# Kernel tuning notes

Measured on AMD Instinct MI355X. Metric: run time of the kernel, lower is better.

Reference implementation:

```python
import jax, jax.numpy as jnp
import numpy as np

# ---- JPEG constants ----
_Y_TABLE = np.array([
    [16, 11, 10, 16, 24, 40, 51, 61],
    [12, 12, 14, 19, 26, 58, 60, 55],
    [14, 13, 16, 24, 40, 57, 69, 56],
    [14, 17, 22, 29, 51, 87, 80, 62],
    [18, 22, 37, 56, 68, 109, 103, 77],
    [24, 35, 55, 64, 81, 104, 113, 92],
    [49, 64, 78, 87, 103, 121, 120, 101],
    [72, 92, 95, 98, 112, 100, 103, 99]], dtype=np.float32)
_C_TABLE = np.full((8, 8), 99.0, dtype=np.float32)
_C_TABLE[:4, :4] = np.array([
    [17, 18, 24, 47],
    [18, 21, 26, 66],
    [24, 26, 56, 99],
    [47, 66, 99, 99]], dtype=np.float32)

_i = np.arange(8, dtype=np.float64)
_T = (np.cos((2 * _i[:, None, None, None] + 1) * _i[None, None, :, None] * np.pi / 16)
      * np.cos((2 * _i[None, :, None, None] + 1) * _i[None, None, None, :] * np.pi / 16))
_alpha = np.ones(8); _alpha[0] = 1.0 / np.sqrt(2.0)
DCT_T = jnp.asarray(_T, jnp.float32)
DCT_SCALE = jnp.asarray(np.outer(_alpha, _alpha) * 0.25, jnp.float32)
IDCT_ALPHA = jnp.asarray(np.outer(_alpha, _alpha), jnp.float32)
Y_T = jnp.asarray(_Y_TABLE)
C_T = jnp.asarray(_C_TABLE)


def _split_blocks(c):
    # [N,H,W] -> [N, (H//8)*(W//8), 8, 8]
    N, H, W = c.shape
    return c.reshape(N, H // 8, 8, W // 8, 8).transpose(0, 1, 3, 2, 4).reshape(N, -1, 8, 8)


def _merge_blocks(b, H, W):
    N = b.shape[0]
    return b.reshape(N, H // 8, W // 8, 8, 8).transpose(0, 1, 3, 2, 4).reshape(N, H, W)


def _dct8x8(b):
    return DCT_SCALE * jnp.einsum('nbxy,xyuv->nbuv', b - 128.0, DCT_T)


def _idct8x8(b):
    return 0.25 * jnp.einsum('nbuv,xyuv->nbxy', b * IDCT_ALPHA, DCT_T) + 128.0


def _diff_round(x):
    r = jnp.round(x)
    return r + (x - r) ** 3


def _quality_to_factor(q):
    return (5000.0 / q if q < 50 else 200.0 - 2.0 * q) / 100.0


def _diff_jpeg(x, quality=99.0):
    # x: [N,3,16,16] roughly in [0,1]
    factor = _quality_to_factor(quality)
    img = x * 255.0
    M = jnp.array([[0.299, 0.587, 0.114],
                   [-0.168736, -0.331264, 0.5],
                   [0.5, -0.418688, -0.081312]], jnp.float32)
    shift = jnp.array([0.0, 128.0, 128.0], jnp.float32)
    ycc = jnp.einsum('nchw,kc->nkhw', img, M) + shift[None, :, None, None]
    y, cb, cr = ycc[:, 0], ycc[:, 1], ycc[:, 2]
    N, H, W = y.shape
    sub = lambda c: c.reshape(N, H // 2, 2, W // 2, 2).mean(axis=(2, 4))  # 2x2 chroma subsample

    def codec(c, tab):
        q = _diff_round(_dct8x8(_split_blocks(c)) / (tab * factor))
        return _idct8x8(q * (tab * factor))

    y2 = _merge_blocks(codec(y, Y_T), H, W)
    up = lambda c: jnp.repeat(jnp.repeat(c, 2, axis=1), 2, axis=2)
    cb2 = up(_merge_blocks(codec(sub(cb), C_T), H // 2, W // 2))
    cr2 = up(_merge_blocks(codec(sub(cr), C_T), H // 2, W // 2))
    ycc2 = jnp.stack([y2, cb2, cr2], axis=1)
    Mi = jnp.array([[1.0, 0.0, 1.402],
                    [1.0, -0.344136, -0.714136],
                    [1.0, 1.772, 0.0]], jnp.float32)
    shift2 = jnp.array([0.0, -128.0, -128.0], jnp.float32)
    rgb = jnp.einsum('nkhw,ck->nchw', ycc2 + shift2[None, :, None, None], Mi)
    return jnp.clip(rgb, 0.0, 255.0) / 255.0


def setup_inputs() -> dict:
    key = jax.random.key(0)
    x = jax.random.normal(key, (32, 1024, 14, 14), dtype=jnp.float32)
    return {"x": x}


def reference(x):
    orig_min = jnp.min(x, axis=(-2, -1), keepdims=True)
    orig_max = jnp.max(x, axis=(-2, -1), keepdims=True)
    rng = orig_max - orig_min + 1e-5
    xn = (x - orig_min) / rng
    B, C, H, W = x.shape
    # replicate each channel into a 3-channel image
    xr = jnp.broadcast_to(xn[:, :, None], (B, C, 3, H, W)).reshape(B * C, 3, H, W)
    xp = jnp.pad(xr, ((0, 0), (0, 0), (1, 1), (1, 1)), mode='edge')  # 14x14 -> 16x16
    comp = _diff_jpeg(xp, 99.0)
    comp = comp[:, :, 1:-1, 1:-1].reshape(B, C, 3, H, W).mean(axis=2)
    return comp * rng + orig_min
```

## Files before the change

kernel.cpp:

```cpp
#include <hip/hip_runtime.h>


namespace {

constexpr int CH_PER_WG = 8;
constexpr int HW        = 196;
constexpr int CS        = 288;
constexpr int WREG      = 2 * CS;

constexpr float CM[8][8] = {
  { 0.35355339059327376f,  0.35355339059327376f,  0.35355339059327376f,  0.35355339059327376f,
    0.35355339059327376f,  0.35355339059327376f,  0.35355339059327376f,  0.35355339059327376f},
  { 0.49039264020161522f,  0.41573480615127262f,  0.27778511650980114f,  0.09754516100806417f,
   -0.09754516100806417f, -0.27778511650980114f, -0.41573480615127262f, -0.49039264020161522f},
  { 0.46193976625564337f,  0.19134171618254492f, -0.19134171618254492f, -0.46193976625564337f,
   -0.46193976625564337f, -0.19134171618254492f,  0.19134171618254492f,  0.46193976625564337f},
  { 0.41573480615127262f, -0.09754516100806417f, -0.49039264020161522f, -0.27778511650980114f,
    0.27778511650980114f,  0.49039264020161522f,  0.09754516100806417f, -0.41573480615127262f},
  { 0.35355339059327376f, -0.35355339059327376f, -0.35355339059327376f,  0.35355339059327376f,
    0.35355339059327376f, -0.35355339059327376f, -0.35355339059327376f,  0.35355339059327376f},
  { 0.27778511650980114f, -0.49039264020161522f,  0.09754516100806417f,  0.41573480615127262f,
   -0.41573480615127262f, -0.09754516100806417f,  0.49039264020161522f, -0.27778511650980114f},
  { 0.19134171618254492f, -0.46193976625564337f,  0.46193976625564337f, -0.19134171618254492f,
   -0.19134171618254492f,  0.46193976625564337f, -0.46193976625564337f,  0.19134171618254492f},
  { 0.09754516100806417f, -0.27778511650980114f,  0.41573480615127262f, -0.49039264020161522f,
    0.49039264020161522f, -0.41573480615127262f,  0.27778511650980114f, -0.09754516100806417f},
};

}

__device__ const float YQTAB[8][8] = {
  {16,11,10,16,24,40,51,61},
  {12,12,14,19,26,58,60,55},
  {14,13,16,24,40,57,69,56},
  {14,17,22,29,51,87,80,62},
  {18,22,37,56,68,109,103,77},
  {24,35,55,64,81,104,113,92},
  {49,64,78,87,103,121,120,101},
  {72,92,95,98,112,100,103,99},
};

#define WAVE_LDS_SYNC() asm volatile("s_waitcnt lgkmcnt(0)" ::: "memory")
#define WAVE_VM_SYNC()  asm volatile("s_waitcnt vmcnt(0)" ::: "memory")

typedef __attribute__((address_space(1))) const void gvoid_t;
typedef __attribute__((address_space(3))) void       lvoid_t;

__global__ __launch_bounds__(256)
void jpeg_codec_kernel(const float* __restrict__ x, float* __restrict__ out) {
  __shared__ __align__(16) float s_A[CH_PER_WG * CS];
  __shared__ __align__(16) float s_B[CH_PER_WG * CS];

  const int tid = threadIdx.x;
  const int w   = tid >> 6;
  const int wl  = tid & 63;
  const int chl = (tid >> 5) & 1;
  const int l   = tid & 31;

  const long long g4 = (long long)blockIdx.x * (CH_PER_WG * HW / 4) + w * (2 * HW / 4);

  {
    const float4* x4 = (const float4*)x + g4;
    float* raw = s_A + w * WREG;
    __builtin_amdgcn_global_load_lds((gvoid_t*)(x4 + wl), (lvoid_t*)raw, 16, 0, 0);
    if (wl < 2 * HW / 4 - 64)
      __builtin_amdgcn_global_load_lds((gvoid_t*)(x4 + 64 + wl),
                                       (lvoid_t*)(raw + 256), 16, 0, 0);
  }
  WAVE_VM_SYNC();

  const float* raw_ch = s_A + w * WREG + chl * HW;

  float mn, inv;
  float mn0, mn1, sc0, sc1;
  {
    float vmin = 1e30f, vmax = -1e30f;
    const float4* c4 = (const float4*)raw_ch;
    {
      float4 v = c4[l];
      vmin = fminf(fminf(vmin, v.x), fminf(v.y, fminf(v.z, v.w)));
      vmax = fmaxf(fmaxf(vmax, v.x), fmaxf(v.y, fmaxf(v.z, v.w)));
    }
    if (l < 17) {
      float4 v = c4[l + 32];
      vmin = fminf(fminf(vmin, v.x), fminf(v.y, fminf(v.z, v.w)));
      vmax = fmaxf(fmaxf(vmax, v.x), fmaxf(v.y, fmaxf(v.z, v.w)));
    }
    #pragma unroll
    for (int off = 16; off; off >>= 1) {
      vmin = fminf(vmin, __shfl_xor(vmin, off, 64));
      vmax = fmaxf(vmax, __shfl_xor(vmax, off, 64));
    }
    mn = vmin;
    float rng   = vmax - vmin + 1e-5f;
    inv         = 255.0f / rng;
    float scale = rng * (1.0f / 255.0f);
    mn0 = __shfl(mn, 0, 64);  mn1 = __shfl(mn, 32, 64);
    sc0 = __shfl(scale, 0, 64); sc1 = __shfl(scale, 32, 64);
  }

  const int b = l >> 3;
  const int i = l & 7;
  const int cbase = w * WREG + chl * CS;
  const int rbase = cbase + b * 72 + i * 9;
  const int wbase = cbase + b * 72 + i;

  float m[8];

  {
    const int pr = ((b >> 1) << 3) + i;
    int sr = pr - 1; sr = sr < 0 ? 0 : (sr > 13 ? 13 : sr);
    const float* rp = raw_ch + sr * 14;
    #pragma unroll
    for (int j = 0; j < 8; ++j) {
      int pc = ((b & 1) << 3) + j - 1; pc = pc < 0 ? 0 : (pc > 13 ? 13 : pc);
      m[j] = fmaf(rp[pc] - mn, inv, -128.0f);
    }
    #pragma unroll
    for (int k = 0; k < 8; ++k) {
      float s = 0.0f;
      #pragma unroll
      for (int j = 0; j < 8; ++j) s = fmaf(m[j], CM[k][j], s);
      s_B[wbase + 9 * k] = s;
    }
  }
  WAVE_LDS_SYNC();

  #pragma unroll
  for (int j = 0; j < 8; ++j) m[j] = s_B[rbase + j];
  #pragma unroll
  for (int k = 0; k < 8; ++k) {
    float s = 0.0f;
    #pragma unroll
    for (int j = 0; j < 8; ++j) s = fmaf(m[j], CM[k][j], s);
    float qv = YQTAB[k][i] * 0.02f;
    float xq = s / qv;
    float r  = rintf(xq);
    float e  = xq - r;
    s_A[wbase + 9 * k] = (r + e * e * e) * qv;
  }
  WAVE_LDS_SYNC();

  #pragma unroll
  for (int j = 0; j < 8; ++j) m[j] = s_A[rbase + j];
  #pragma unroll
  for (int k = 0; k < 8; ++k) {
    float s = 0.0f;
    #pragma unroll
    for (int j = 0; j < 8; ++j) s = fmaf(m[j], CM[j][k], s);
    s_B[wbase + 9 * k] = s;
  }
  WAVE_LDS_SYNC();

  #pragma unroll
  for (int j = 0; j < 8; ++j) m[j] = s_B[rbase + j];
  #pragma unroll
  for (int k = 0; k < 8; ++k) {
    float s = 0.0f;
    #pragma unroll
    for (int j = 0; j < 8; ++j) s = fmaf(m[j], CM[j][k], s);
    s_A[wbase + 9 * k] = s;
  }
  WAVE_LDS_SYNC();

  {
    float4* o4 = (float4*)out + g4;
    #pragma unroll
    for (int k = 0; k < 2; ++k) {
      int t = wl + k * 64;
      if (t < 2 * HW / 4) {
        int idx = 4 * t;
        int c2l = idx / HW;
        int rem = idx - c2l * HW;
        int r0  = rem / 14, c0 = rem - 14 * r0;
        float cmn = c2l ? mn1 : mn0;
        float csc = c2l ? sc1 : sc0;
        const float* blk = s_A + w * WREG + c2l * CS;
        float vals[4];
        #pragma unroll
        for (int q = 0; q < 4; ++q) {
          int rr = r0, cc = c0 + q;
          if (cc >= 14) { cc -= 14; ++rr; }
          int pr = rr + 1, pc = cc + 1;
          int bb = ((pr >> 3) << 1) | (pc >> 3);
          float v = blk[bb * 72 + (pr & 7) * 9 + (pc & 7)] + 128.0f;
          v = v < 0.0f ? 0.0f : (v > 255.0f ? 255.0f : v);
          vals[q] = fmaf(v, csc, cmn);
        }
        o4[t] = make_float4(vals[0], vals[1], vals[2], vals[3]);
      }
    }
  }
}

extern "C" void kernel_launch(void* const* d_in, const int* in_sizes, int n_in,
                              void* d_out, int out_size, void* d_ws, size_t ws_size,
                              hipStream_t stream) {
  const float* x = (const float*)d_in[0];
  float* out     = (float*)d_out;
  const int ntot = in_sizes[0];
  const int nch  = ntot / HW;
  const int grid = (nch + CH_PER_WG - 1) / CH_PER_WG;
  hipLaunchKernelGGL(jpeg_codec_kernel, dim3(grid), dim3(256), 0, stream,
                     x, out);
}
```

Before: 83.57 us.

## Fuse crop, clamp and denormalize into final IDCT pass and store contiguously

After: 81.44 us. 2.6% less time.

```diff
diff --git a/kernel.cpp b/kernel.cpp
--- a/kernel.cpp
+++ b/kernel.cpp
@@ -29,16 +29,18 @@
 
 }
 
-__device__ const float YQTAB[8][8] = {
-  {16,11,10,16,24,40,51,61},
-  {12,12,14,19,26,58,60,55},
-  {14,13,16,24,40,57,69,56},
-  {14,17,22,29,51,87,80,62},
-  {18,22,37,56,68,109,103,77},
-  {24,35,55,64,81,104,113,92},
-  {49,64,78,87,103,121,120,101},
-  {72,92,95,98,112,100,103,99},
+#define SF 0.02f
+__device__ __align__(16) const float QVT[8][8] = {
+  {16*SF, 12*SF, 14*SF, 14*SF, 18*SF,  24*SF,  49*SF,  72*SF},
+  {11*SF, 12*SF, 13*SF, 17*SF, 22*SF,  35*SF,  64*SF,  92*SF},
+  {10*SF, 14*SF, 16*SF, 22*SF, 37*SF,  55*SF,  78*SF,  95*SF},
+  {16*SF, 19*SF, 24*SF, 29*SF, 56*SF,  64*SF,  87*SF,  98*SF},
+  {24*SF, 26*SF, 40*SF, 51*SF, 68*SF,  81*SF, 103*SF, 112*SF},
+  {40*SF, 58*SF, 57*SF, 87*SF, 109*SF, 104*SF, 121*SF, 100*SF},
+  {51*SF, 60*SF, 69*SF, 80*SF, 103*SF, 113*SF, 120*SF, 103*SF},
+  {61*SF, 55*SF, 56*SF, 62*SF, 77*SF,  92*SF, 101*SF,  99*SF},
 };
+#undef SF
 
 #define WAVE_LDS_SYNC() asm volatile("s_waitcnt lgkmcnt(0)" ::: "memory")
 #define WAVE_VM_SYNC()  asm volatile("s_waitcnt vmcnt(0)" ::: "memory")
@@ -46,7 +48,7 @@
 typedef __attribute__((address_space(1))) const void gvoid_t;
 typedef __attribute__((address_space(3))) void       lvoid_t;
 
-__global__ __launch_bounds__(256)
+__global__ __launch_bounds__(256, 8)
 void jpeg_codec_kernel(const float* __restrict__ x, float* __restrict__ out) {
   __shared__ __align__(16) float s_A[CH_PER_WG * CS];
   __shared__ __align__(16) float s_B[CH_PER_WG * CS];
@@ -67,12 +69,23 @@
       __builtin_amdgcn_global_load_lds((gvoid_t*)(x4 + 64 + wl),
                                        (lvoid_t*)(raw + 256), 16, 0, 0);
   }
+
+  const int b = l >> 3;
+  const int i = l & 7;
+
+  float qv8[8];
+  {
+    const float4* qt = (const float4*)QVT[i];
+    float4 qa = qt[0], qb = qt[1];
+    qv8[0] = qa.x; qv8[1] = qa.y; qv8[2] = qa.z; qv8[3] = qa.w;
+    qv8[4] = qb.x; qv8[5] = qb.y; qv8[6] = qb.z; qv8[7] = qb.w;
+  }
+
   WAVE_VM_SYNC();
 
   const float* raw_ch = s_A + w * WREG + chl * HW;
 
-  float mn, inv;
-  float mn0, mn1, sc0, sc1;
+  float mn, inv, scale;
   {
     float vmin = 1e30f, vmax = -1e30f;
     const float4* c4 = (const float4*)raw_ch;
@@ -92,15 +105,11 @@
       vmax = fmaxf(vmax, __shfl_xor(vmax, off, 64));
     }
     mn = vmin;
-    float rng   = vmax - vmin + 1e-5f;
-    inv         = 255.0f / rng;
-    float scale = rng * (1.0f / 255.0f);
-    mn0 = __shfl(mn, 0, 64);  mn1 = __shfl(mn, 32, 64);
-    sc0 = __shfl(scale, 0, 64); sc1 = __shfl(scale, 32, 64);
-  }
-
-  const int b = l >> 3;
-  const int i = l & 7;
+    float rng = vmax - vmin + 1e-5f;
+    inv   = 255.0f / rng;
+    scale = rng * (1.0f / 255.0f);
+  }
+
   const int cbase = w * WREG + chl * CS;
   const int rbase = cbase + b * 72 + i * 9;
   const int wbase = cbase + b * 72 + i;
@@ -133,7 +142,7 @@
     float s = 0.0f;
     #pragma unroll
     for (int j = 0; j < 8; ++j) s = fmaf(m[j], CM[k][j], s);
-    float qv = YQTAB[k][i] * 0.02f;
+    float qv = qv8[k];
     float xq = s / qv;
     float r  = rintf(xq);
     float e  = xq - r;
@@ -152,44 +161,34 @@
   }
   WAVE_LDS_SYNC();
 
-  #pragma unroll
-  for (int j = 0; j < 8; ++j) m[j] = s_B[rbase + j];
-  #pragma unroll
-  for (int k = 0; k < 8; ++k) {
-    float s = 0.0f;
-    #pragma unroll
-    for (int j = 0; j < 8; ++j) s = fmaf(m[j], CM[j][k], s);
-    s_A[wbase + 9 * k] = s;
-  }
-  WAVE_LDS_SYNC();
-
-  {
+  {
+    #pragma unroll
+    for (int j = 0; j < 8; ++j) m[j] = s_B[rbase + j];
+    const int pc    = ((b & 1) << 3) + i;
+    const int prb   = (b >> 1) << 3;
+    const bool pcv  = (pc >= 1) && (pc <= 14);
+    const int obase = prb * 14 + pc - 15;
+    float* crop = s_A + w * WREG + chl * HW;
+    #pragma unroll
+    for (int k = 0; k < 8; ++k) {
+      float s = 0.0f;
+      #pragma unroll
+      for (int j = 0; j < 8; ++j) s = fmaf(m[j], CM[j][k], s);
+      const int pr = prb + k;
+      if (pcv && pr >= 1 && pr <= 14) {
+        float v = fminf(fmaxf(s + 128.0f, 0.0f), 255.0f);
+        crop[obase + 14 * k] = fmaf(v, scale, mn);
+      }
+    }
+  }
+  WAVE_LDS_SYNC();
+
+  {
+    const float4* src = (const float4*)(s_A + w * WREG);
     float4* o4 = (float4*)out + g4;
-    #pragma unroll
-    for (int k = 0; k < 2; ++k) {
-      int t = wl + k * 64;
-      if (t < 2 * HW / 4) {
-        int idx = 4 * t;
-        int c2l = idx / HW;
-        int rem = idx - c2l * HW;
-        int r0  = rem / 14, c0 = rem - 14 * r0;
-        float cmn = c2l ? mn1 : mn0;
-        float csc = c2l ? sc1 : sc0;
-        const float* blk = s_A + w * WREG + c2l * CS;
-        float vals[4];
-        #pragma unroll
-        for (int q = 0; q < 4; ++q) {
-          int rr = r0, cc = c0 + q;
-          if (cc >= 14) { cc -= 14; ++rr; }
-          int pr = rr + 1, pc = cc + 1;
-          int bb = ((pr >> 3) << 1) | (pc >> 3);
-          float v = blk[bb * 72 + (pr & 7) * 9 + (pc & 7)] + 128.0f;
-          v = v < 0.0f ? 0.0f : (v > 255.0f ? 255.0f : v);
-          vals[q] = fmaf(v, csc, cmn);
-        }
-        o4[t] = make_float4(vals[0], vals[1], vals[2], vals[3]);
-      }
-    }
+    o4[wl] = src[wl];
+    if (wl < 2 * HW / 4 - 64)
+      o4[64 + wl] = src[64 + wl];
   }
 }
 
```
